# Kernel tuning notes

Measured on AMD Instinct MI355X. Metric: run time of the kernel, lower is better.

## Reference

```python
import jax, jax.numpy as jnp
import numpy as np

D_MODEL = 1024
N_HEADS = 16
WINDOW = 256
SSM_N = 256
EPS = 1e-5


def _layernorm(x, g, b):
    m = x.mean(-1, keepdims=True)
    v = ((x - m) ** 2).mean(-1, keepdims=True)
    return (x - m) / jnp.sqrt(v + EPS) * g + b


def _sliding_window_attn(Q, K, V, W):
    # Q,K,V: [B,h,T,dh]; exact sliding-window causal attention (keys q-W+1..q)
    B, h, T, dh = Q.shape
    nb = T // W
    Qb = Q.reshape(B, h, nb, W, dh)
    pad = jnp.zeros((B, h, W, dh), Q.dtype)
    Kp = jnp.concatenate([pad, K], axis=2)  # [B,h,T+W,dh]
    Kprev = Kp[:, :, :T].reshape(B, h, nb, W, dh)
    Kcur = K.reshape(B, h, nb, W, dh)
    Kwin = jnp.concatenate([Kprev, Kcur], axis=3)  # [B,h,nb,2W,dh]
    Vp = jnp.concatenate([pad, V], axis=2)
    Vprev = Vp[:, :, :T].reshape(B, h, nb, W, dh)
    Vcur = V.reshape(B, h, nb, W, dh)
    Vwin = jnp.concatenate([Vprev, Vcur], axis=3)
    scores = jnp.einsum('bhnid,bhnjd->bhnij', Qb, Kwin) / jnp.sqrt(jnp.asarray(dh, Q.dtype))
    i = jnp.arange(W)[:, None]
    j = jnp.arange(2 * W)[None, :]
    blk = jnp.arange(nb)[:, None, None]
    # key global pos = blk*W - W + j ; valid iff i < j <= i+W and key pos >= 0
    mask = (j > i) & (j <= i + W) & (blk * W - W + j >= 0)  # [nb,W,2W]
    neg = jnp.asarray(jnp.finfo(scores.dtype).min, scores.dtype)
    scores = jnp.where(mask[None, None], scores, neg)
    p = jax.nn.softmax(scores, axis=-1)
    out = jnp.einsum('bhnij,bhnjd->bhnid', p, Vwin)
    return out.reshape(B, h, T, dh)


def _forward(x, ssm_state, ln1_g, ln1_b, ln2_g, ln2_b, wq, bq, wk, bk, wv, bv,
             wo, bo, wg, bg, A, Bw, Cw, w1, b1, w2, b2):
    B, T, d = x.shape
    h = N_HEADS
    dh = d // h
    xn = _layernorm(x, ln1_g, ln1_b)
    # windowed attention path
    Q = (xn @ wq + bq).reshape(B, T, h, dh).transpose(0, 2, 1, 3)
    K = (xn @ wk + bk).reshape(B, T, h, dh).transpose(0, 2, 1, 3)
    V = (xn @ wv + bv).reshape(B, T, h, dh).transpose(0, 2, 1, 3)
    ao = _sliding_window_attn(Q, K, V, WINDOW)
    y_attn = ao.transpose(0, 2, 1, 3).reshape(B, T, d) @ wo + bo
    # SSM path: s_t = tanh(A)*s_{t-1} + B x_t ; y_t = C s_t
    alpha = jnp.tanh(A)
    u = xn @ Bw  # [B,T,N]
    def step(s, u_t):
        s = alpha * s + u_t
        return s, s
    new_state, states = jax.lax.scan(step, ssm_state, u.transpose(1, 0, 2))
    y_ssm = states.transpose(1, 0, 2) @ Cw  # [B,T,d]
    # gated fusion + residual
    g = jax.nn.sigmoid(xn @ wg + bg)
    y = g * y_attn + (1.0 - g) * y_ssm
    x = x + y
    # Pre-LN MLP
    x2 = _layernorm(x, ln2_g, ln2_b)
    x = x + jax.nn.gelu(x2 @ w1 + b1, approximate=False) @ w2 + b2
    return x, new_state


def setup_inputs() -> dict:
    key = jax.random.key(0)
    ks = jax.random.split(key, 16)
    B, T, d, N = 2, 2048, D_MODEL, SSM_N
    s = 0.02
    inp = {
        'x': jax.random.normal(ks[0], (B, T, d), jnp.float32),
        'ssm_state': jnp.zeros((B, N), jnp.float32),
        'ln1_g': jnp.ones((d,), jnp.float32),
        'ln1_b': jnp.zeros((d,), jnp.float32),
        'ln2_g': jnp.ones((d,), jnp.float32),
        'ln2_b': jnp.zeros((d,), jnp.float32),
        'wq': jax.random.normal(ks[1], (d, d), jnp.float32) * s,
        'bq': jnp.zeros((d,), jnp.float32),
        'wk': jax.random.normal(ks[2], (d, d), jnp.float32) * s,
        'bk': jnp.zeros((d,), jnp.float32),
        'wv': jax.random.normal(ks[3], (d, d), jnp.float32) * s,
        'bv': jnp.zeros((d,), jnp.float32),
        'wo': jax.random.normal(ks[4], (d, d), jnp.float32) * s,
        'bo': jnp.zeros((d,), jnp.float32),
        'wg': jax.random.normal(ks[5], (d, d), jnp.float32) * s,
        'bg': jnp.zeros((d,), jnp.float32),
        'A': jax.random.uniform(ks[6], (N,), jnp.float32, -0.1, 0.1),
        'Bw': jax.random.normal(ks[7], (d, N), jnp.float32) * s,
        'Cw': jax.random.normal(ks[8], (N, d), jnp.float32) * s,
        'w1': jax.random.normal(ks[9], (d, 4 * d), jnp.float32) * s,
        'b1': jnp.zeros((4 * d,), jnp.float32),
        'w2': jax.random.normal(ks[10], (4 * d, d), jnp.float32) * s,
        'b2': jnp.zeros((d,), jnp.float32),
    }
    return inp


def reference(x, ssm_state, ln1_g, ln1_b, ln2_g, ln2_b, wq, bq, wk, bk, wv, bv,
              wo, bo, wg, bg, A, Bw, Cw, w1, b1, w2, b2):
    return _forward(x, ssm_state, ln1_g, ln1_b, ln2_g, ln2_b, wq, bq, wk, bk,
                    wv, bv, wo, bo, wg, bg, A, Bw, Cw, w1, b1, w2, b2)
```

## Files before the change

kernel.cpp:

```cpp
#include <hip/hip_runtime.h>
#include <math.h>

#define BB 2
#define TT 2048
#define DD 1024
#define HH 16
#define DH 64
#define WW 256
#define NN 256
#define ROWS (BB*TT)
#define ROWSZ ((size_t)ROWS*DD)
#define NQU 4352

typedef unsigned short u16;
typedef __attribute__((ext_vector_type(8))) short short8;
typedef __attribute__((ext_vector_type(4))) float f32x4;

__device__ __forceinline__ float bf2f(u16 h) {
    union { unsigned int u; float f; } c; c.u = ((unsigned int)h) << 16; return c.f;
}
__device__ __forceinline__ u16 f2bf(float f) {
    union { float f; unsigned int u; } c; c.f = f;
    unsigned int r = c.u + 0x7fffu + ((c.u >> 16) & 1u);
    return (u16)(r >> 16);
}

__device__ __forceinline__ void gld16(const void* g, void* l) {
    __builtin_amdgcn_global_load_lds(
        (const __attribute__((address_space(1))) void*)g,
        (__attribute__((address_space(3))) void*)l, 16, 0, 0);
}

__global__ __launch_bounds__(256) void ln_kernel(const float* __restrict__ x,
                                                 const float* __restrict__ g,
                                                 const float* __restrict__ b,
                                                 u16* __restrict__ out) {
    int row = blockIdx.x;
    int t = threadIdx.x;
    const float4* xr = (const float4*)(x + (size_t)row * DD);
    float4 v4 = xr[t];
    float s  = v4.x + v4.y + v4.z + v4.w;
    float s2 = v4.x*v4.x + v4.y*v4.y + v4.z*v4.z + v4.w*v4.w;
    #pragma unroll
    for (int o = 32; o > 0; o >>= 1) { s += __shfl_xor(s, o); s2 += __shfl_xor(s2, o); }
    __shared__ float red[2][4];
    int wid = t >> 6, lane = t & 63;
    if (lane == 0) { red[0][wid] = s; red[1][wid] = s2; }
    __syncthreads();
    s  = red[0][0] + red[0][1] + red[0][2] + red[0][3];
    s2 = red[1][0] + red[1][1] + red[1][2] + red[1][3];
    float mean = s * (1.0f / DD);
    float var  = s2 * (1.0f / DD) - mean * mean;
    float inv  = rsqrtf(var + 1e-5f);
    const float4* g4 = (const float4*)g;
    const float4* b4 = (const float4*)b;
    float4 gg = g4[t], bb = b4[t];
    float o0 = (v4.x - mean) * inv * gg.x + bb.x;
    float o1 = (v4.y - mean) * inv * gg.y + bb.y;
    float o2 = (v4.z - mean) * inv * gg.z + bb.z;
    float o3 = (v4.w - mean) * inv * gg.w + bb.w;
    uint2 packed;
    packed.x = (unsigned)f2bf(o0) | ((unsigned)f2bf(o1) << 16);
    packed.y = (unsigned)f2bf(o2) | ((unsigned)f2bf(o3) << 16);
    *(uint2*)(out + (size_t)row * DD + 4 * t) = packed;
}

__global__ __launch_bounds__(256) void tconv_all(
    const float* __restrict__ wq, const float* __restrict__ wk,
    const float* __restrict__ wv, const float* __restrict__ wg,
    const float* __restrict__ Bw, const float* __restrict__ wo,
    const float* __restrict__ Cw, const float* __restrict__ w1,
    const float* __restrict__ w2,
    u16* __restrict__ wqkvgut, u16* __restrict__ wot, u16* __restrict__ cwt,
    u16* __restrict__ w1t, u16* __restrict__ w2t) {
    int tile = blockIdx.x;
    const float* src; u16* dst; int K, N, tx, ty;
    if (tile < 4096) {
        int seg = tile >> 10, tl = tile & 1023;
        src = (seg == 0) ? wq : (seg == 1) ? wk : (seg == 2) ? wv : wg;
        dst = wqkvgut + (size_t)seg * 1024 * 1024;
        K = 1024; N = 1024; tx = tl & 31; ty = tl >> 5;
    } else if (tile < 4352) {
        int tl = tile - 4096;
        src = Bw; dst = wqkvgut + (size_t)4096 * 1024;
        K = 1024; N = 256; tx = tl & 7; ty = tl >> 3;
    } else if (tile < 5376) {
        int tl = tile - 4352;
        src = wo; dst = wot; K = 1024; N = 1024; tx = tl & 31; ty = tl >> 5;
    } else if (tile < 5632) {
        int tl = tile - 5376;
        src = Cw; dst = cwt; K = 256; N = 1024; tx = tl & 31; ty = tl >> 5;
    } else if (tile < 9728) {
        int tl = tile - 5632;
        src = w1; dst = w1t; K = 1024; N = 4096; tx = tl & 127; ty = tl >> 7;
    } else {
        int tl = tile - 9728;
        src = w2; dst = w2t; K = 4096; N = 1024; tx = tl & 31; ty = tl >> 5;
    }
    __shared__ float ts[32][33];
    int n0 = tx * 32, k0 = ty * 32;
    int tc = threadIdx.x & 31, tr = threadIdx.x >> 5;
    #pragma unroll
    for (int i = tr; i < 32; i += 8)
        ts[i][tc] = src[(size_t)(k0 + i) * N + n0 + tc];
    __syncthreads();
    #pragma unroll
    for (int i = tr; i < 32; i += 8)
        dst[(size_t)(n0 + i) * K + k0 + tc] = f2bf(ts[tc][i]);
}

__global__ __launch_bounds__(256) void bias_init(const float* __restrict__ bq,
                                                 const float* __restrict__ bk,
                                                 const float* __restrict__ bv,
                                                 const float* __restrict__ bg,
                                                 float* __restrict__ dst) {
    int i = blockIdx.x * 256 + threadIdx.x;
    if (i >= NQU) return;
    float v = 0.f;
    if (i < 1024) v = bq[i];
    else if (i < 2048) v = bk[i - 1024];
    else if (i < 3072) v = bv[i - 2048];
    else if (i < 4096) v = bg[i - 3072];
    dst[i] = v;
}

#define TILEB 32768

__device__ __forceinline__ void gemm_core_8ph(const u16* __restrict__ A,
                                              const u16* __restrict__ Bt,
                                              int K, int kiters, int kofs,
                                              int m0, int n0,
                                              char* Als, char* Bls,
                                              int t, f32x4 acc[8][4]) {
    int lane = t & 63, wid = t >> 6;
    int wm = wid >> 2, wn = wid & 3;
    int jq = lane >> 4, rq = lane & 15;
    int csw0 = (jq ^ (rq & 7)) << 4;
    int csw1 = ((4 + jq) ^ (rq & 7)) << 4;
    int rowB[4];
    #pragma unroll
    for (int jn = 0; jn < 4; jn++) rowB[jn] = (wn * 64 + jn * 16 + rq) * 128;
    int rowA[8];
    #pragma unroll
    for (int i = 0; i < 8; i++) rowA[i] = (i * 32 + wm * 16 + rq) * 128;

    int r0 = t >> 3, p8 = t & 7;
    int jg = p8 ^ (r0 & 7);
    const char* gAb = (const char*)(A + (size_t)(m0 + r0) * K + kofs) + jg * 16;
    const char* gBb = (const char*)(Bt + (size_t)(n0 + r0) * K + kofs) + jg * 16;
    size_t st64 = (size_t)K * 128;
    int ldst = t * 16;

    #pragma unroll
    for (int q = 0; q < 4; q++) gld16(gBb + q * st64, Bls + q * 8192 + ldst);
    #pragma unroll
    for (int q = 0; q < 4; q++) gld16(gAb + q * st64, Als + q * 8192 + ldst);
    asm volatile("s_waitcnt vmcnt(0)" ::: "memory");
    __builtin_amdgcn_s_barrier();

    short8 bfr[4][2];

#define MFMA_SET(P) \
    __builtin_amdgcn_s_setprio(1); \
    _Pragma("unroll") \
    for (int ii = 0; ii < 2; ii++) { \
        _Pragma("unroll") \
        for (int jn = 0; jn < 4; jn++) { \
            acc[2*(P)+ii][jn] = __builtin_amdgcn_mfma_f32_16x16x32_bf16(af[ii][0], bfr[jn][0], acc[2*(P)+ii][jn], 0, 0, 0); \
            acc[2*(P)+ii][jn] = __builtin_amdgcn_mfma_f32_16x16x32_bf16(af[ii][1], bfr[jn][1], acc[2*(P)+ii][jn], 0, 0, 0); \
        } \
    } \
    __builtin_amdgcn_s_setprio(0); \
    __builtin_amdgcn_s_barrier();

    for (int kt = 0; kt < kiters; kt++) {
        int cur = kt & 1, nxt = cur ^ 1;
        bool nl = (kt + 1 < kiters);
        size_t kn = (size_t)(kt + 1) * 128;
        const char* Ab = Als + cur * TILEB;
        const char* Bb = Bls + cur * TILEB;
        char* An = Als + nxt * TILEB;
        char* Bn = Bls + nxt * TILEB;

        {
            short8 af[2][2];
            #pragma unroll
            for (int ii = 0; ii < 2; ii++) {
                af[ii][0] = *(const short8*)(Ab + rowA[ii] + csw0);
                af[ii][1] = *(const short8*)(Ab + rowA[ii] + csw1);
            }
            #pragma unroll
            for (int jn = 0; jn < 4; jn++) {
                bfr[jn][0] = *(const short8*)(Bb + rowB[jn] + csw0);
                bfr[jn][1] = *(const short8*)(Bb + rowB[jn] + csw1);
            }
            if (nl) {
                gld16(gBb + kn, Bn + ldst);
                gld16(gBb + kn + st64, Bn + 8192 + ldst);
                asm volatile("s_waitcnt vmcnt(4)" ::: "memory");
            } else {
                asm volatile("s_waitcnt vmcnt(2)" ::: "memory");
            }
            __builtin_amdgcn_s_barrier();
            MFMA_SET(0)
        }
        {
            short8 af[2][2];
            #pragma unroll
            for (int ii = 0; ii < 2; ii++) {
                af[ii][0] = *(const short8*)(Ab + rowA[2+ii] + csw0);
                af[ii][1] = *(const short8*)(Ab + rowA[2+ii] + csw1);
            }
            if (nl) {
                gld16(gBb + kn + 2*st64, Bn + 2*8192 + ldst);
                gld16(gBb + kn + 3*st64, Bn + 3*8192 + ldst);
                asm volatile("s_waitcnt vmcnt(5)" ::: "memory");
            } else {
                asm volatile("s_waitcnt vmcnt(1)" ::: "memory");
            }
            __builtin_amdgcn_s_barrier();
            MFMA_SET(1)
        }
        {
            short8 af[2][2];
            #pragma unroll
            for (int ii = 0; ii < 2; ii++) {
                af[ii][0] = *(const short8*)(Ab + rowA[4+ii] + csw0);
                af[ii][1] = *(const short8*)(Ab + rowA[4+ii] + csw1);
            }
            if (nl) {
                gld16(gAb + kn, An + ldst);
                gld16(gAb + kn + st64, An + 8192 + ldst);
                asm volatile("s_waitcnt vmcnt(6)" ::: "memory");
            } else {
                asm volatile("s_waitcnt vmcnt(0)" ::: "memory");
            }
            __builtin_amdgcn_s_barrier();
            MFMA_SET(2)
        }
        {
            short8 af[2][2];
            #pragma unroll
            for (int ii = 0; ii < 2; ii++) {
                af[ii][0] = *(const short8*)(Ab + rowA[6+ii] + csw0);
                af[ii][1] = *(const short8*)(Ab + rowA[6+ii] + csw1);
            }
            if (nl) {
                gld16(gAb + kn + 2*st64, An + 2*8192 + ldst);
                gld16(gAb + kn + 3*st64, An + 3*8192 + ldst);
                asm volatile("s_waitcnt vmcnt(3)" ::: "memory");
            }
            __builtin_amdgcn_s_barrier();
            MFMA_SET(3)
        }
    }
#undef MFMA_SET
}

template<int ACT, bool OUTBF, bool SPLIT>
__global__ __launch_bounds__(512, 2) void mgemm64(const u16* __restrict__ A,
                                                  const u16* __restrict__ Bt,
                                                  const float* __restrict__ bias,
                                                  void* __restrict__ C,
                                                  int M, int N, int K, int Kslice,
                                                  int mtiles, int ntiles, int PM, int PN) {
    __shared__ __align__(16) char Als[2 * TILEB];
    __shared__ __align__(16) char Bls[2 * TILEB];
    int t = threadIdx.x;
    int l = blockIdx.x;
    int xcd = l & 7, li = l >> 3;
    int rm = mtiles / PM, rn = ntiles / PN;
    int xm = xcd % PM, xn = xcd / PM;
    int mt = xm * rm + li % rm;
    int nt = xn * rn + li / rm;
    int m0 = mt * 256, n0 = nt * 256;
    int z = SPLIT ? blockIdx.y : 0;
    f32x4 acc[8][4];
    #pragma unroll
    for (int i = 0; i < 8; i++)
        #pragma unroll
        for (int j = 0; j < 4; j++)
            acc[i][j] = (f32x4){0.f, 0.f, 0.f, 0.f};
    gemm_core_8ph(A, Bt, K, Kslice >> 6, z * Kslice, m0, n0, Als, Bls, t, acc);

    int lane = t & 63, wid = t >> 6;
    int wm = wid >> 2, wn = wid & 3;
    int jq = lane >> 4, rq = lane & 15;
    u16* Cb = OUTBF ? ((u16*)C + (SPLIT ? (size_t)z * M * N : (size_t)0)) : nullptr;
    float* Cf = (float*)C;
    #pragma unroll
    for (int i = 0; i < 8; i++) {
        int rowb = m0 + i * 32 + wm * 16 + jq * 4;
        #pragma unroll
        for (int jn = 0; jn < 4; jn++) {
            int col = n0 + wn * 64 + jn * 16 + rq;
            float bv = bias ? bias[col] : 0.f;
            #pragma unroll
            for (int rr = 0; rr < 4; rr++) {
                float v = acc[i][jn][rr] + bv;
                if (ACT == 1) v = 0.5f * v * (1.0f + erff(v * 0.70710678118654752f));
                size_t off = (size_t)(rowb + rr) * N + col;
                if (OUTBF) Cb[off] = f2bf(v);
                else Cf[off] = v;
            }
        }
    }
}

__global__ __launch_bounds__(512, 2) void proj3(const u16* __restrict__ ao,
                                                const u16* __restrict__ states,
                                                const u16* __restrict__ wot,
                                                const u16* __restrict__ cwt,
                                                const float* __restrict__ bo,
                                                u16* __restrict__ ya0,
                                                u16* __restrict__ ya1,
                                                float* __restrict__ ys) {
    __shared__ __align__(16) char Als[2 * TILEB];
    __shared__ __align__(16) char Bls[2 * TILEB];
    int t = threadIdx.x;
    int m0 = blockIdx.y * 256, n0 = blockIdx.x * 256;
    int z = blockIdx.z;
    const u16* A; const u16* Bt; int K, kofs, kiters;
    if (z < 2) { A = ao; Bt = wot; K = 1024; kofs = z * 512; kiters = 8; }
    else       { A = states; Bt = cwt; K = 256; kofs = 0; kiters = 4; }
    f32x4 acc[8][4];
    #pragma unroll
    for (int i = 0; i < 8; i++)
        #pragma unroll
        for (int j = 0; j < 4; j++)
            acc[i][j] = (f32x4){0.f, 0.f, 0.f, 0.f};
    gemm_core_8ph(A, Bt, K, kiters, kofs, m0, n0, Als, Bls, t, acc);

    int lane = t & 63, wid = t >> 6;
    int wm = wid >> 2, wn = wid & 3;
    int jq = lane >> 4, rq = lane & 15;
    u16* dst = (z == 0) ? ya0 : ya1;
    #pragma unroll
    for (int i = 0; i < 8; i++) {
        int rowb = m0 + i * 32 + wm * 16 + jq * 4;
        #pragma unroll
        for (int jn = 0; jn < 4; jn++) {
            int col = n0 + wn * 64 + jn * 16 + rq;
            float bv = (z == 0) ? bo[col] : 0.f;
            #pragma unroll
            for (int rr = 0; rr < 4; rr++) {
                float v = acc[i][jn][rr] + bv;
                size_t off = (size_t)(rowb + rr) * DD + col;
                if (z < 2) dst[off] = f2bf(v);
                else ys[off] = v;
            }
        }
    }
}

__global__ __launch_bounds__(256) void attn_scan(const u16* __restrict__ QKVG,
                                                 u16* __restrict__ O,
                                                 const float* __restrict__ Assm,
                                                 const float* __restrict__ s0,
                                                 u16* __restrict__ states,
                                                 float* __restrict__ s_out) {
    __shared__ __align__(16) short Qs[8][64][8];
    __shared__ __align__(16) short Ks[8][64][8];
    __shared__ __align__(16) short Vt[64][72];
    __shared__ __align__(16) short Ps[4][16][72];

    if (blockIdx.x >= 1024) {
        int idx = (blockIdx.x - 1024) * 256 + threadIdx.x;
        int n = idx & 255;
        int c = (idx >> 8) & 31;
        int b = idx >> 13;
        float alpha = tanhf(Assm[n]);
        int t0 = c * 64;
        float s = (c == 0) ? s0[b * NN + n] : 0.f;
        const u16* up = QKVG + (size_t)(b * TT) * NQU + 4096 + n;
        if (c > 0) {
            #pragma unroll
            for (int k = 8; k >= 1; k--)
                s = alpha * s + bf2f(up[(size_t)(t0 - k) * NQU]);
        }
        u16* sp = states + (size_t)(b * TT) * NN + n;
        for (int t = t0; t < t0 + 64; t++) {
            s = alpha * s + bf2f(up[(size_t)t * NQU]);
            sp[(size_t)t * NN] = f2bf(s);
        }
        if (c == 31) s_out[b * NN + n] = s;
        return;
    }

    int blk = blockIdx.x;
    int qb = blk & 31;
    int h  = (blk >> 5) & 15;
    int b  = blk >> 9;
    int q0 = qb * 64;
    int t = threadIdx.x, lane = t & 63, w = t >> 6;
    int rq = lane & 15, jq = lane >> 4;

    const size_t RS = NQU;

    #pragma unroll
    for (int i = 0; i < 2; i++) {
        int c = 2 * w + i;
        const u16* g = QKVG + (size_t)(b * TT + q0 + lane) * RS + h * 64 + c * 8;
        gld16(g, (char*)Qs + c * 1024);
    }

    f32x4 Oa[4];
    #pragma unroll
    for (int tj = 0; tj < 4; tj++) Oa[tj] = (f32x4){0.f, 0.f, 0.f, 0.f};
    float mrow[4], lrow[4];
    #pragma unroll
    for (int r = 0; r < 4; r++) { mrow[r] = -1e30f; lrow[r] = 0.f; }

    int c0 = 4 - (q0 >> 6); if (c0 < 0) c0 = 0;

    for (int ci = c0; ci < 5; ci++) {
        int kbase = q0 - 256 + ci * 64;
        #pragma unroll
        for (int i = 0; i < 2; i++) {
            int c = 2 * w + i;
            const u16* g = QKVG + (size_t)(b * TT + kbase + lane) * RS + 1024 + h * 64 + c * 8;
            gld16(g, (char*)Ks + c * 1024);
        }
        #pragma unroll
        for (int i = 0; i < 2; i++) {
            int dhg = i * 4 + w;
            uint4 v = *(const uint4*)(QKVG + (size_t)(b * TT + kbase + lane) * RS + 2048 + h * 64 + dhg * 8);
            const u16* pv = (const u16*)&v;
            #pragma unroll
            for (int j = 0; j < 8; j++) Vt[dhg * 8 + j][lane] = (short)pv[j];
        }
        __syncthreads();

        short8 qf[2];
        #pragma unroll
        for (int s = 0; s < 2; s++)
            qf[s] = *(const short8*)&Qs[4 * s + jq][w * 16 + rq][0];

        f32x4 S[4];
        #pragma unroll
        for (int tj = 0; tj < 4; tj++) S[tj] = (f32x4){0.f, 0.f, 0.f, 0.f};
        #pragma unroll
        for (int s = 0; s < 2; s++)
            #pragma unroll
            for (int tj = 0; tj < 4; tj++) {
                short8 kf = *(const short8*)&Ks[4 * s + jq][tj * 16 + rq][0];
                S[tj] = __builtin_amdgcn_mfma_f32_16x16x32_bf16(qf[s], kf, S[tj], 0, 0, 0);
            }

        #pragma unroll
        for (int r = 0; r < 4; r++) {
            int q = q0 + w * 16 + jq * 4 + r;
            float sv[4];
            #pragma unroll
            for (int tj = 0; tj < 4; tj++) {
                int kp = kbase + tj * 16 + rq;
                float x = S[tj][r] * 0.125f;
                bool valid = (kp <= q) && (kp > q - WW);
                sv[tj] = valid ? x : -1e30f;
            }
            float cm = fmaxf(fmaxf(sv[0], sv[1]), fmaxf(sv[2], sv[3]));
            #pragma unroll
            for (int o = 1; o < 16; o <<= 1) cm = fmaxf(cm, __shfl_xor(cm, o));
            float mn = fmaxf(mrow[r], cm);
            bool any = mn > -1e29f;
            float al = any ? __expf(mrow[r] - mn) : 1.f;
            float ps = 0.f;
            #pragma unroll
            for (int tj = 0; tj < 4; tj++) {
                float p = any ? __expf(sv[tj] - mn) : 0.f;
                ps += p;
                Ps[w][jq * 4 + r][tj * 16 + rq] = (short)f2bf(p);
            }
            #pragma unroll
            for (int o = 1; o < 16; o <<= 1) ps += __shfl_xor(ps, o);
            lrow[r] = lrow[r] * al + ps;
            mrow[r] = mn;
            #pragma unroll
            for (int tj = 0; tj < 4; tj++) Oa[tj][r] *= al;
        }

        #pragma unroll
        for (int s = 0; s < 2; s++) {
            short8 pf = *(const short8*)&Ps[w][rq][32 * s + 8 * jq];
            #pragma unroll
            for (int tj = 0; tj < 4; tj++) {
                short8 vf = *(const short8*)&Vt[tj * 16 + rq][32 * s + 8 * jq];
                Oa[tj] = __builtin_amdgcn_mfma_f32_16x16x32_bf16(pf, vf, Oa[tj], 0, 0, 0);
            }
        }
        __syncthreads();
    }

    #pragma unroll
    for (int r = 0; r < 4; r++) {
        int q = q0 + w * 16 + jq * 4 + r;
        float inv = 1.f / lrow[r];
        #pragma unroll
        for (int tj = 0; tj < 4; tj++)
            O[(size_t)(b * TT + q) * DD + h * 64 + tj * 16 + rq] = f2bf(Oa[tj][r] * inv);
    }
}

__global__ __launch_bounds__(256) void fuse_ln2(const float* __restrict__ x,
                                                const u16* __restrict__ QKVG,
                                                const u16* __restrict__ ya0,
                                                const u16* __restrict__ ya1,
                                                const float* __restrict__ ys,
                                                const float* __restrict__ g2,
                                                const float* __restrict__ b2,
                                                float* __restrict__ out,
                                                u16* __restrict__ x2n) {
    int row = blockIdx.x, t = threadIdx.x;
    float4 xv = ((const float4*)(x + (size_t)row * DD))[t];
    uint2 gw = *(const uint2*)(QKVG + (size_t)row * NQU + 3072 + 4 * t);
    uint2 a0 = *(const uint2*)(ya0 + (size_t)row * DD + 4 * t);
    uint2 a1 = *(const uint2*)(ya1 + (size_t)row * DD + 4 * t);
    float4 sv = ((const float4*)(ys + (size_t)row * DD))[t];
    u16 gh[4] = {(u16)(gw.x & 0xffff), (u16)(gw.x >> 16), (u16)(gw.y & 0xffff), (u16)(gw.y >> 16)};
    u16 ah[4] = {(u16)(a0.x & 0xffff), (u16)(a0.x >> 16), (u16)(a0.y & 0xffff), (u16)(a0.y >> 16)};
    u16 bh[4] = {(u16)(a1.x & 0xffff), (u16)(a1.x >> 16), (u16)(a1.y & 0xffff), (u16)(a1.y >> 16)};
    float xe[4] = {xv.x, xv.y, xv.z, xv.w};
    float se[4] = {sv.x, sv.y, sv.z, sv.w};
    float o[4];
    #pragma unroll
    for (int e = 0; e < 4; e++) {
        float g = 1.0f / (1.0f + __expf(-bf2f(gh[e])));
        float a = bf2f(ah[e]) + bf2f(bh[e]);
        o[e] = xe[e] + g * a + (1.0f - g) * se[e];
    }
    float s = o[0] + o[1] + o[2] + o[3];
    float s2 = o[0]*o[0] + o[1]*o[1] + o[2]*o[2] + o[3]*o[3];
    #pragma unroll
    for (int off = 32; off > 0; off >>= 1) { s += __shfl_xor(s, off); s2 += __shfl_xor(s2, off); }
    __shared__ float red[2][4];
    int wid = t >> 6, lane = t & 63;
    if (lane == 0) { red[0][wid] = s; red[1][wid] = s2; }
    __syncthreads();
    s  = red[0][0] + red[0][1] + red[0][2] + red[0][3];
    s2 = red[1][0] + red[1][1] + red[1][2] + red[1][3];
    float mean = s * (1.0f / DD);
    float var  = s2 * (1.0f / DD) - mean * mean;
    float inv  = rsqrtf(var + 1e-5f);
    float4 gg = ((const float4*)g2)[t];
    float4 bb = ((const float4*)b2)[t];
    float ge[4] = {gg.x, gg.y, gg.z, gg.w};
    float be[4] = {bb.x, bb.y, bb.z, bb.w};
    float4 ov = {o[0], o[1], o[2], o[3]};
    ((float4*)(out + (size_t)row * DD))[t] = ov;
    u16 nh[4];
    #pragma unroll
    for (int e = 0; e < 4; e++) nh[e] = f2bf((o[e] - mean) * inv * ge[e] + be[e]);
    uint2 packed;
    packed.x = (unsigned)nh[0] | ((unsigned)nh[1] << 16);
    packed.y = (unsigned)nh[2] | ((unsigned)nh[3] << 16);
    *(uint2*)(x2n + (size_t)row * DD + 4 * t) = packed;
}

__global__ __launch_bounds__(256) void mlp2_reduce(const u16* __restrict__ pbase,
                                                   const float* __restrict__ b2,
                                                   float* __restrict__ out) {
    size_t i4 = (size_t)blockIdx.x * 256 + threadIdx.x;
    float4 o = ((float4*)out)[i4];
    float4 bb = ((const float4*)b2)[i4 & 255];
    float acc0 = bb.x, acc1 = bb.y, acc2 = bb.z, acc3 = bb.w;
    #pragma unroll
    for (int z = 0; z < 4; z++) {
        uint2 p = ((const uint2*)(pbase + (size_t)z * ROWSZ))[i4];
        acc0 += bf2f((u16)(p.x & 0xffff));
        acc1 += bf2f((u16)(p.x >> 16));
        acc2 += bf2f((u16)(p.y & 0xffff));
        acc3 += bf2f((u16)(p.y >> 16));
    }
    o.x += acc0; o.y += acc1; o.z += acc2; o.w += acc3;
    ((float4*)out)[i4] = o;
}

extern "C" void kernel_launch(void* const* d_in, const int* in_sizes, int n_in,
                              void* d_out, int out_size, void* d_ws, size_t ws_size,
                              hipStream_t stream) {
    const float* x     = (const float*)d_in[0];
    const float* sst   = (const float*)d_in[1];
    const float* ln1g  = (const float*)d_in[2];
    const float* ln1b  = (const float*)d_in[3];
    const float* ln2g  = (const float*)d_in[4];
    const float* ln2b  = (const float*)d_in[5];
    const float* wq    = (const float*)d_in[6];
    const float* bq    = (const float*)d_in[7];
    const float* wk    = (const float*)d_in[8];
    const float* bk    = (const float*)d_in[9];
    const float* wv    = (const float*)d_in[10];
    const float* bv    = (const float*)d_in[11];
    const float* wo    = (const float*)d_in[12];
    const float* bo    = (const float*)d_in[13];
    const float* wg    = (const float*)d_in[14];
    const float* bg    = (const float*)d_in[15];
    const float* A     = (const float*)d_in[16];
    const float* Bw    = (const float*)d_in[17];
    const float* Cw    = (const float*)d_in[18];
    const float* w1    = (const float*)d_in[19];
    const float* b1    = (const float*)d_in[20];
    const float* w2    = (const float*)d_in[21];
    const float* b2    = (const float*)d_in[22];

    float* out = (float*)d_out;
    char* ws = (char*)d_ws;
    const size_t KBs = 1024;

    u16*   QKVGU  = (u16*)(ws);
    u16*   ya0b   = (u16*)(ws + 34816 * KBs);
    u16*   ya1b   = (u16*)(ws + 43008 * KBs);
    float* ys     = (float*)(ws + 51200 * KBs);
    u16*   parts  = ya0b;
    u16*   xn     = (u16*)(ws + 67584 * KBs);
    u16*   ao     = (u16*)(ws + 75776 * KBs);
    u16*   states = (u16*)(ws + 83968 * KBs);
    u16*   wqkvgut= (u16*)(ws + 86016 * KBs);
    u16*   wot    = (u16*)(ws + 94720 * KBs);
    u16*   cwt    = (u16*)(ws + 96768 * KBs);
    u16*   w1t    = (u16*)(ws + 97280 * KBs);
    u16*   w2t    = (u16*)(ws + 105472 * KBs);
    float* biasq  = (float*)(ws + 113664 * KBs);
    u16*   x2n    = xn;
    u16*   h1     = QKVGU;

    float* new_state_out = out + ROWSZ;

    hipLaunchKernelGGL(tconv_all, dim3(13824), dim3(256), 0, stream,
                       wq, wk, wv, wg, Bw, wo, Cw, w1, w2,
                       wqkvgut, wot, cwt, w1t, w2t);
    hipLaunchKernelGGL(bias_init, dim3(17), dim3(256), 0, stream, bq, bk, bv, bg, biasq);

    hipLaunchKernelGGL(ln_kernel, dim3(ROWS), dim3(256), 0, stream, x, ln1g, ln1b, xn);
    hipLaunchKernelGGL((mgemm64<0,true,false>), dim3(272, 1), dim3(512), 0, stream,
                       xn, wqkvgut, biasq, (void*)QKVGU, ROWS, NQU, 1024, 1024,
                       16, 17, 8, 1);
    hipLaunchKernelGGL(attn_scan, dim3(1088), dim3(256), 0, stream,
                       QKVGU, ao, A, sst, states, new_state_out);
    hipLaunchKernelGGL(proj3, dim3(4, 16, 3), dim3(512), 0, stream,
                       ao, states, wot, cwt, bo, ya0b, ya1b, ys);
    hipLaunchKernelGGL(fuse_ln2, dim3(ROWS), dim3(256), 0, stream,
                       x, QKVGU, ya0b, ya1b, ys, ln2g, ln2b, out, x2n);
    hipLaunchKernelGGL((mgemm64<1,true,false>), dim3(256, 1), dim3(512), 0, stream,
                       x2n, w1t, b1, (void*)h1, ROWS, 4*DD, 1024, 1024,
                       16, 16, 4, 2);
    hipLaunchKernelGGL((mgemm64<0,true,true>), dim3(64, 4), dim3(512), 0, stream,
                       h1, w2t, (const float*)nullptr, (void*)parts, ROWS, DD, 4096, 1024,
                       16, 4, 8, 1);
    hipLaunchKernelGGL(mlp2_reduce, dim3(4096), dim3(256), 0, stream, parts, b2, out);
}
```

Measured before the change: 407.8 us.

## Split SSM input projection out of fused QKVG GEMM into split-K GEMM plus reduce

The fused projection GEMM no longer includes the 256 SSM input columns (N goes from 4352 to 4096), so its grid drops from 17 column tiles to 16 with a different tile mapping. The u = xn @ Bw product is now computed by a separate split-K GEMM writing four bf16 partials, which a new ureduce kernel sums into a compact [rows,256] buffer. The scan then reads u with a 256-element stride instead of the 4352-wide row, which should improve its memory locality. In exchange it adds two launches, an extra partial write/read round trip, and bf16 rounding of the split-K partials. It also reuses the xn buffer to hold u.

```diff
diff --git a/kernel.cpp b/kernel.cpp
--- a/kernel.cpp
+++ b/kernel.cpp
@@ -10,7 +10,6 @@
 #define NN 256
 #define ROWS (BB*TT)
 #define ROWSZ ((size_t)ROWS*DD)
-#define NQU 4352
 
 typedef unsigned short u16;
 typedef __attribute__((ext_vector_type(8))) short short8;
@@ -115,12 +114,12 @@
                                                  const float* __restrict__ bg,
                                                  float* __restrict__ dst) {
     int i = blockIdx.x * 256 + threadIdx.x;
-    if (i >= NQU) return;
-    float v = 0.f;
+    if (i >= 4096) return;
+    float v;
     if (i < 1024) v = bq[i];
     else if (i < 2048) v = bk[i - 1024];
     else if (i < 3072) v = bv[i - 2048];
-    else if (i < 4096) v = bg[i - 3072];
+    else v = bg[i - 3072];
     dst[i] = v;
 }
 
@@ -307,6 +306,24 @@
     }
 }
 
+__global__ __launch_bounds__(256) void ureduce(const u16* __restrict__ p,
+                                               u16* __restrict__ o) {
+    size_t i2 = (size_t)blockIdx.x * 256 + threadIdx.x;
+    float a0 = 0.f, a1 = 0.f, a2 = 0.f, a3 = 0.f;
+    #pragma unroll
+    for (int z = 0; z < 4; z++) {
+        uint2 v = ((const uint2*)(p + (size_t)z * 1048576))[i2];
+        a0 += bf2f((u16)(v.x & 0xffff));
+        a1 += bf2f((u16)(v.x >> 16));
+        a2 += bf2f((u16)(v.y & 0xffff));
+        a3 += bf2f((u16)(v.y >> 16));
+    }
+    uint2 r;
+    r.x = (unsigned)f2bf(a0) | ((unsigned)f2bf(a1) << 16);
+    r.y = (unsigned)f2bf(a2) | ((unsigned)f2bf(a3) << 16);
+    ((uint2*)o)[i2] = r;
+}
+
 __global__ __launch_bounds__(512, 2) void proj3(const u16* __restrict__ ao,
                                                 const u16* __restrict__ states,
                                                 const u16* __restrict__ wot,
@@ -354,6 +371,7 @@
 }
 
 __global__ __launch_bounds__(256) void attn_scan(const u16* __restrict__ QKVG,
+                                                 const u16* __restrict__ ubuf,
                                                  u16* __restrict__ O,
                                                  const float* __restrict__ Assm,
                                                  const float* __restrict__ s0,
@@ -372,15 +390,15 @@
         float alpha = tanhf(Assm[n]);
         int t0 = c * 64;
         float s = (c == 0) ? s0[b * NN + n] : 0.f;
-        const u16* up = QKVG + (size_t)(b * TT) * NQU + 4096 + n;
+        const u16* up = ubuf + (size_t)(b * TT) * NN + n;
         if (c > 0) {
             #pragma unroll
             for (int k = 8; k >= 1; k--)
-                s = alpha * s + bf2f(up[(size_t)(t0 - k) * NQU]);
+                s = alpha * s + bf2f(up[(size_t)(t0 - k) * NN]);
         }
         u16* sp = states + (size_t)(b * TT) * NN + n;
         for (int t = t0; t < t0 + 64; t++) {
-            s = alpha * s + bf2f(up[(size_t)t * NQU]);
+            s = alpha * s + bf2f(up[(size_t)t * NN]);
             sp[(size_t)t * NN] = f2bf(s);
         }
         if (c == 31) s_out[b * NN + n] = s;
@@ -395,7 +413,7 @@
     int t = threadIdx.x, lane = t & 63, w = t >> 6;
     int rq = lane & 15, jq = lane >> 4;
 
-    const size_t RS = NQU;
+    const size_t RS = 4096;
 
     #pragma unroll
     for (int i = 0; i < 2; i++) {
@@ -512,7 +530,7 @@
                                                 u16* __restrict__ x2n) {
     int row = blockIdx.x, t = threadIdx.x;
     float4 xv = ((const float4*)(x + (size_t)row * DD))[t];
-    uint2 gw = *(const uint2*)(QKVG + (size_t)row * NQU + 3072 + 4 * t);
+    uint2 gw = *(const uint2*)(QKVG + (size_t)row * 4096 + 3072 + 4 * t);
     uint2 a0 = *(const uint2*)(ya0 + (size_t)row * DD + 4 * t);
     uint2 a1 = *(const uint2*)(ya1 + (size_t)row * DD + 4 * t);
     float4 sv = ((const float4*)(ys + (size_t)row * DD))[t];
@@ -606,10 +624,11 @@
     char* ws = (char*)d_ws;
     const size_t KBs = 1024;
 
-    u16*   QKVGU  = (u16*)(ws);
+    u16*   QKVG   = (u16*)(ws);
     u16*   ya0b   = (u16*)(ws + 34816 * KBs);
     u16*   ya1b   = (u16*)(ws + 43008 * KBs);
     float* ys     = (float*)(ws + 51200 * KBs);
+    u16*   uparts = ya0b;
     u16*   parts  = ya0b;
     u16*   xn     = (u16*)(ws + 67584 * KBs);
     u16*   ao     = (u16*)(ws + 75776 * KBs);
@@ -621,25 +640,31 @@
     u16*   w2t    = (u16*)(ws + 105472 * KBs);
     float* biasq  = (float*)(ws + 113664 * KBs);
     u16*   x2n    = xn;
-    u16*   h1     = QKVGU;
+    u16*   ubuf   = xn;
+    u16*   h1     = QKVG;
 
     float* new_state_out = out + ROWSZ;
 
     hipLaunchKernelGGL(tconv_all, dim3(13824), dim3(256), 0, stream,
                        wq, wk, wv, wg, Bw, wo, Cw, w1, w2,
                        wqkvgut, wot, cwt, w1t, w2t);
-    hipLaunchKernelGGL(bias_init, dim3(17), dim3(256), 0, stream, bq, bk, bv, bg, biasq);
+    hipLaunchKernelGGL(bias_init, dim3(16), dim3(256), 0, stream, bq, bk, bv, bg, biasq);
 
     hipLaunchKernelGGL(ln_kernel, dim3(ROWS), dim3(256), 0, stream, x, ln1g, ln1b, xn);
-    hipLaunchKernelGGL((mgemm64<0,true,false>), dim3(272, 1), dim3(512), 0, stream,
-                       xn, wqkvgut, biasq, (void*)QKVGU, ROWS, NQU, 1024, 1024,
-                       16, 17, 8, 1);
+    hipLaunchKernelGGL((mgemm64<0,true,false>), dim3(256, 1), dim3(512), 0, stream,
+                       xn, wqkvgut, biasq, (void*)QKVG, ROWS, 4096, 1024, 1024,
+                       16, 16, 4, 2);
+    hipLaunchKernelGGL((mgemm64<0,true,true>), dim3(16, 4), dim3(512), 0, stream,
+                       xn, wqkvgut + (size_t)4096 * 1024, (const float*)nullptr,
+                       (void*)uparts, ROWS, 256, 1024, 256,
+                       16, 1, 8, 1);
+    hipLaunchKernelGGL(ureduce, dim3(1024), dim3(256), 0, stream, uparts, ubuf);
     hipLaunchKernelGGL(attn_scan, dim3(1088), dim3(256), 0, stream,
-                       QKVGU, ao, A, sst, states, new_state_out);
+                       QKVG, ubuf, ao, A, sst, states, new_state_out);
     hipLaunchKernelGGL(proj3, dim3(4, 16, 3), dim3(512), 0, stream,
                        ao, states, wot, cwt, bo, ya0b, ya1b, ys);
     hipLaunchKernelGGL(fuse_ln2, dim3(ROWS), dim3(256), 0, stream,
-                       x, QKVGU, ya0b, ya1b, ys, ln2g, ln2b, out, x2n);
+                       x, QKVG, ya0b, ya1b, ys, ln2g, ln2b, out, x2n);
     hipLaunchKernelGGL((mgemm64<1,true,false>), dim3(256, 1), dim3(512), 0, stream,
                        x2n, w1t, b1, (void*)h1, ROWS, 4*DD, 1024, 1024,
                        16, 16, 4, 2);
```

After: 394.6 us. 3.2% less time.
